# Kernel tuning notes

Measured on AMD Instinct MI355X. Metric: run time of the kernel, lower is better.

## Reference

```python
import jax, jax.numpy as jnp
import numpy as np

N_NODES = 10000
N_EDGES = 320000
IN_DIM = 128
HID = 256


def setup_inputs() -> dict:
    key = jax.random.key(0)
    ks = jax.random.split(key, 10)
    s_in = 1.0 / np.sqrt(IN_DIM)
    s_h = 1.0 / np.sqrt(HID)
    return {
        "x": jax.random.normal(ks[0], (N_NODES, IN_DIM), dtype=jnp.float32),
        "edge_index": jax.random.randint(ks[1], (2, N_EDGES), 0, N_NODES, dtype=jnp.int64),
        # feature_projector Linear(IN_DIM -> HID)
        "Wp": jax.random.uniform(ks[2], (IN_DIM, HID), jnp.float32, -s_in, s_in),
        "bp": jax.random.uniform(ks[3], (HID,), jnp.float32, -s_in, s_in),
        # LSTM(input=HID, hidden=HID) params, torch layout [4H, H], gate order i,f,g,o
        "W_ih": jax.random.uniform(ks[4], (4 * HID, HID), jnp.float32, -s_h, s_h),
        "W_hh": jax.random.uniform(ks[5], (4 * HID, HID), jnp.float32, -s_h, s_h),
        "b_ih": jax.random.uniform(ks[6], (4 * HID,), jnp.float32, -s_h, s_h),
        "b_hh": jax.random.uniform(ks[7], (4 * HID,), jnp.float32, -s_h, s_h),
        # EvolveGCN-O initial weight [H, H] (glorot-style)
        "initial_weight": jax.random.normal(ks[8], (HID, HID), dtype=jnp.float32) * np.sqrt(2.0 / (2 * HID)),
        # GCNConv bias
        "b_gcn": jnp.zeros((HID,), dtype=jnp.float32),
    }


def _forward(x, edge_index, Wp, bp, W_ih, W_hh, b_ih, b_hh, initial_weight, b_gcn):
    n = x.shape[0]
    # 1) feature projection
    h = x @ Wp + bp  # [N, H]
    # 2) EvolveGCN-O: one LSTM step on the weight matrix (rows = batch),
    #    with h0 = c0 = initial_weight; evolved hidden state is the GCN weight.
    gates = initial_weight @ W_ih.T + b_ih + initial_weight @ W_hh.T + b_hh  # [H, 4H]
    i_g, f_g, g_g, o_g = jnp.split(gates, 4, axis=-1)
    c = jax.nn.sigmoid(f_g) * initial_weight + jax.nn.sigmoid(i_g) * jnp.tanh(g_g)
    W = jax.nn.sigmoid(o_g) * jnp.tanh(c)  # [H, H]
    # 3) GCN propagation with fixed W: out = D^{-1/2}(A+I)D^{-1/2} (h W) + b
    hw = h @ W  # [N, H]
    self_loop = jnp.arange(n, dtype=edge_index.dtype)
    src = jnp.concatenate([edge_index[0], self_loop])
    dst = jnp.concatenate([edge_index[1], self_loop])
    ones = jnp.ones(src.shape[0], dtype=hw.dtype)
    deg = jax.ops.segment_sum(ones, dst, num_segments=n)  # in-degree incl. self loop
    dinv = jnp.where(deg > 0, jax.lax.rsqrt(deg), 0.0)
    norm = dinv[src] * dinv[dst]  # [E+N]
    out = jax.ops.segment_sum(hw[src] * norm[:, None], dst, num_segments=n)
    return out + b_gcn


def reference(x, edge_index, Wp, bp, W_ih, W_hh, b_ih, b_hh, initial_weight, b_gcn):
    return _forward(x, edge_index, Wp, bp, W_ih, W_hh, b_ih, b_hh, initial_weight, b_gcn)
```

## Files before the change

kernel.cpp:

```cpp
#include <hip/hip_runtime.h>
#include <math.h>

#define N_NODES 10000
#define N_EDGES 320000
#define IN_DIM  128
#define HID     256
#define CAP     128
#define NWB     64
#define NXB     128
#define NFB     448
#define NBB     (NXB + NFB)

typedef __attribute__((ext_vector_type(8))) short frag_ab;
typedef __attribute__((ext_vector_type(4))) float frag_cd;


__device__ __forceinline__ unsigned bf16rne(float f) {
    union { float f; unsigned u; } c; c.f = f;
    return (c.u + 0x7FFFu + ((c.u >> 16) & 1u)) >> 16;
}
__device__ __forceinline__ float sig_f(float x)  { return 1.f / (1.f + __expf(-x)); }
__device__ __forceinline__ float tanh_f(float x) { return 1.f - 2.f / (1.f + __expf(2.f * x)); }

__global__ __launch_bounds__(256, 2)
void k_w(const float* __restrict__ Wp, const float* __restrict__ bp,
         const float* __restrict__ wih, const float* __restrict__ whh,
         const float* __restrict__ b_ih, const float* __restrict__ b_hh,
         const float* __restrict__ iw,
         unsigned* __restrict__ wct, float* __restrict__ bc) {
    __shared__ __align__(16) char smem_raw[57920];
    const int bid = blockIdx.x;
    const int t = threadIdx.x;

    float (*aT)[260]  = (float(*)[260])smem_raw;
    float (*bSt)[20]  = (float(*)[20])(smem_raw + 33280);
    float (*iwc)[260] = (float(*)[260])(smem_raw + 53760);
    #pragma unroll
    for (int n = 0; n < 16; ++n) {
        int nrow = (n >> 2) * 256 + 4 * bid + (n & 3);
        bSt[t][n] = wih[nrow * 256 + t] + whh[nrow * 256 + t];
    }
    const int mg = t >> 2, ng = t & 3;
    const int srow = t >> 3, sf4 = t & 7;
    float acc[4][4] = {};
    for (int kt = 0; kt < 8; ++kt) {
        int k0 = kt * 32;
        __syncthreads();
        #pragma unroll
        for (int rr = 0; rr < 8; ++rr) {
            int row = srow + 32 * rr;
            float4 v = *(const float4*)&iw[row * 256 + k0 + 4 * sf4];
            aT[4 * sf4 + 0][row] = v.x; aT[4 * sf4 + 1][row] = v.y;
            aT[4 * sf4 + 2][row] = v.z; aT[4 * sf4 + 3][row] = v.w;
        }
        __syncthreads();
        if (kt == (bid >> 3)) {
            int c0 = (4 * bid) & 31;
            #pragma unroll
            for (int jj = 0; jj < 4; ++jj) iwc[jj][t] = aT[c0 + jj][t];
        }
        #pragma unroll 4
        for (int kk = 0; kk < 32; ++kk) {
            float4 a4 = *(const float4*)&aT[kk][4 * mg];
            float4 b4 = *(const float4*)&bSt[k0 + kk][4 * ng];
            float a[4] = {a4.x, a4.y, a4.z, a4.w};
            float b[4] = {b4.x, b4.y, b4.z, b4.w};
            #pragma unroll
            for (int i = 0; i < 4; ++i)
                #pragma unroll
                for (int j = 0; j < 4; ++j)
                    acc[i][j] = fmaf(a[i], b[j], acc[i][j]);
        }
    }
    float (*gates_lds)[17] = (float(*)[17])smem_raw;
    float (*wevc)[260]     = (float(*)[260])(smem_raw + 33280);
    __syncthreads();
    #pragma unroll
    for (int i = 0; i < 4; ++i)
        #pragma unroll
        for (int j = 0; j < 4; ++j)
            gates_lds[4 * mg + i][4 * ng + j] = acc[i][j];
    __syncthreads();
    {
        int r = t;
        #pragma unroll
        for (int jj = 0; jj < 4; ++jj) {
            int jcol = 4 * bid + jj;
            float gi = gates_lds[r][0  + jj] + b_ih[jcol]       + b_hh[jcol];
            float gf = gates_lds[r][4  + jj] + b_ih[256 + jcol] + b_hh[256 + jcol];
            float gg = gates_lds[r][8  + jj] + b_ih[512 + jcol] + b_hh[512 + jcol];
            float go = gates_lds[r][12 + jj] + b_ih[768 + jcol] + b_hh[768 + jcol];
            float c  = sig_f(gf) * iwc[jj][r] + sig_f(gi) * tanh_f(gg);
            wevc[jj][r] = sig_f(go) * tanh_f(c);
        }
    }
    float (*wpT)[132] = (float(*)[132])smem_raw;
    const int a2 = t & 63, jj = t >> 6;
    float c0 = 0.f, c1 = 0.f;
    for (int kt2 = 0; kt2 < 8; ++kt2) {
        int k0 = kt2 * 32;
        __syncthreads();
        #pragma unroll
        for (int ri = 0; ri < 4; ++ri) {
            int a = srow + 32 * ri;
            float4 v = *(const float4*)&Wp[a * 256 + k0 + 4 * sf4];
            wpT[4 * sf4 + 0][a] = v.x; wpT[4 * sf4 + 1][a] = v.y;
            wpT[4 * sf4 + 2][a] = v.z; wpT[4 * sf4 + 3][a] = v.w;
        }
        __syncthreads();
        #pragma unroll 8
        for (int kk = 0; kk < 32; ++kk) {
            float2 wv = *(const float2*)&wpT[kk][2 * a2];
            float wev = wevc[jj][k0 + kk];
            c0 = fmaf(wv.x, wev, c0);
            c1 = fmaf(wv.y, wev, c1);
        }
    }
    wct[(4 * bid + jj) * 64 + a2] = bf16rne(c0) | (bf16rne(c1) << 16);
    if (t < 4) {
        float s = 0.f;
        #pragma unroll 4
        for (int k4 = 0; k4 < 64; ++k4) {
            float4 b4 = *(const float4*)&bp[4 * k4];
            float4 w4 = *(const float4*)&wevc[t][4 * k4];
            s = fmaf(b4.x, w4.x, fmaf(b4.y, w4.y, fmaf(b4.z, w4.z, fmaf(b4.w, w4.w, s))));
        }
        bc[4 * bid + t] = s;
    }
}

__global__ __launch_bounds__(256)
void k_b(const float* __restrict__ x, const int* __restrict__ ei,
         int* __restrict__ cursor, unsigned* __restrict__ xb,
         int* __restrict__ bucket) {
    const int bid = blockIdx.x;
    const int t = threadIdx.x;
    if (bid < NXB) {
        const float4* x4 = (const float4*)x;
        uint2* xb2 = (uint2*)xb;
        for (int idx = bid * 256 + t; idx < N_NODES * 32; idx += NXB * 256) {
            float4 v = x4[idx];
            xb2[idx] = make_uint2(bf16rne(v.x) | (bf16rne(v.y) << 16),
                                  bf16rne(v.z) | (bf16rne(v.w) << 16));
        }
    } else {
        for (int u = (bid - NXB) * 256 + t; u < N_EDGES / 4; u += NFB * 256) {
            int4 s4 = *(const int4*)&ei[u * 4];
            int4 d4 = *(const int4*)&ei[N_EDGES + u * 4];
            int p0 = atomicAdd(&cursor[d4.x], 1);
            if (p0 < CAP) bucket[d4.x * CAP + p0] = s4.x;
            int p1 = atomicAdd(&cursor[d4.y], 1);
            if (p1 < CAP) bucket[d4.y * CAP + p1] = s4.y;
            int p2 = atomicAdd(&cursor[d4.z], 1);
            if (p2 < CAP) bucket[d4.z * CAP + p2] = s4.z;
            int p3 = atomicAdd(&cursor[d4.w], 1);
            if (p3 < CAP) bucket[d4.w * CAP + p3] = s4.w;
        }
    }
}

__global__ __launch_bounds__(256)
void k_agg(const unsigned* __restrict__ xb, const int* __restrict__ cursor,
           const int* __restrict__ bucket, unsigned* __restrict__ yb,
           float* __restrict__ rs) {
    const int t = threadIdx.x;
    const int wv = t >> 6, lane = t & 63;
    const int v = blockIdx.x * 4 + wv;
    int cntv = cursor[v];
    float dv = rsqrtf((float)(cntv + 1));
    int cnt2 = cntv > CAP ? CAP : cntv;
    unsigned self = xb[v * 64 + lane];
    union { unsigned u; float f; } c0, c1;
    c0.u = self << 16; c1.u = self & 0xFFFF0000u;
    float acc0 = dv * c0.f, acc1 = dv * c1.f, wsum = dv;
    const int4* bkt4 = (const int4*)&bucket[v * CAP];
    int j = 0;
    for (; j + 8 <= cnt2; j += 8) {
        int4 sa = bkt4[j >> 2];
        int4 sb = bkt4[(j >> 2) + 1];
        float w0 = rsqrtf((float)(cursor[sa.x] + 1));
        float w1 = rsqrtf((float)(cursor[sa.y] + 1));
        float w2 = rsqrtf((float)(cursor[sa.z] + 1));
        float w3 = rsqrtf((float)(cursor[sa.w] + 1));
        float w4 = rsqrtf((float)(cursor[sb.x] + 1));
        float w5 = rsqrtf((float)(cursor[sb.y] + 1));
        float w6 = rsqrtf((float)(cursor[sb.z] + 1));
        float w7 = rsqrtf((float)(cursor[sb.w] + 1));
        unsigned r0 = xb[sa.x * 64 + lane];
        unsigned r1 = xb[sa.y * 64 + lane];
        unsigned r2 = xb[sa.z * 64 + lane];
        unsigned r3 = xb[sa.w * 64 + lane];
        unsigned r4 = xb[sb.x * 64 + lane];
        unsigned r5 = xb[sb.y * 64 + lane];
        unsigned r6 = xb[sb.z * 64 + lane];
        unsigned r7 = xb[sb.w * 64 + lane];
        union { unsigned u; float f; } a0, a1;
        a0.u = r0 << 16; a1.u = r0 & 0xFFFF0000u;
        acc0 = fmaf(w0, a0.f, acc0); acc1 = fmaf(w0, a1.f, acc1);
        a0.u = r1 << 16; a1.u = r1 & 0xFFFF0000u;
        acc0 = fmaf(w1, a0.f, acc0); acc1 = fmaf(w1, a1.f, acc1);
        a0.u = r2 << 16; a1.u = r2 & 0xFFFF0000u;
        acc0 = fmaf(w2, a0.f, acc0); acc1 = fmaf(w2, a1.f, acc1);
        a0.u = r3 << 16; a1.u = r3 & 0xFFFF0000u;
        acc0 = fmaf(w3, a0.f, acc0); acc1 = fmaf(w3, a1.f, acc1);
        a0.u = r4 << 16; a1.u = r4 & 0xFFFF0000u;
        acc0 = fmaf(w4, a0.f, acc0); acc1 = fmaf(w4, a1.f, acc1);
        a0.u = r5 << 16; a1.u = r5 & 0xFFFF0000u;
        acc0 = fmaf(w5, a0.f, acc0); acc1 = fmaf(w5, a1.f, acc1);
        a0.u = r6 << 16; a1.u = r6 & 0xFFFF0000u;
        acc0 = fmaf(w6, a0.f, acc0); acc1 = fmaf(w6, a1.f, acc1);
        a0.u = r7 << 16; a1.u = r7 & 0xFFFF0000u;
        acc0 = fmaf(w7, a0.f, acc0); acc1 = fmaf(w7, a1.f, acc1);
        wsum += w0 + w1 + w2 + w3 + w4 + w5 + w6 + w7;
    }
    for (; j < cnt2; ++j) {
        int s = bucket[v * CAP + j];
        float ws = rsqrtf((float)(cursor[s] + 1));
        unsigned rr = xb[s * 64 + lane];
        union { unsigned u; float f; } a0, a1;
        a0.u = rr << 16; a1.u = rr & 0xFFFF0000u;
        acc0 = fmaf(ws, a0.f, acc0); acc1 = fmaf(ws, a1.f, acc1);
        wsum += ws;
    }
    yb[v * 64 + lane] = bf16rne(dv * acc0) | (bf16rne(dv * acc1) << 16);
    if (lane == 0) rs[v] = dv * wsum;
}

__global__ __launch_bounds__(256)
void k_out(const unsigned* __restrict__ yb, const unsigned* __restrict__ wct,
           const float* __restrict__ bc, const float* __restrict__ rs,
           const float* __restrict__ b_gcn, float* __restrict__ out) {
    int m0 = blockIdx.x * 16;
    int w = threadIdx.x >> 6, lane = threadIdx.x & 63;
    int q = lane >> 4, ln = lane & 15;
    const int4* yb4  = (const int4*)yb;
    const int4* wct4 = (const int4*)wct;
    union { int4 v; frag_ab f; } a[4];
    #pragma unroll
    for (int kc = 0; kc < 4; ++kc)
        a[kc].v = yb4[(m0 + ln) * 16 + kc * 4 + q];
    float rsv[4];
    #pragma unroll
    for (int r = 0; r < 4; ++r) rsv[r] = rs[m0 + q * 4 + r];
    #pragma unroll
    for (int i = 0; i < 4; ++i) {
        int n0 = (w + 4 * i) * 16;
        union { int4 v; frag_ab f; } b[4];
        #pragma unroll
        for (int kc = 0; kc < 4; ++kc)
            b[kc].v = wct4[(n0 + ln) * 16 + kc * 4 + q];
        frag_cd acc = {0.f, 0.f, 0.f, 0.f};
        #pragma unroll
        for (int kc = 0; kc < 4; ++kc)
            acc = __builtin_amdgcn_mfma_f32_16x16x32_bf16(a[kc].f, b[kc].f, acc, 0, 0, 0);
        int n = n0 + ln;
        float bcv = bc[n], bgv = b_gcn[n];
        #pragma unroll
        for (int r = 0; r < 4; ++r) {
            int m = m0 + q * 4 + r;
            out[m * HID + n] = acc[r] + rsv[r] * bcv + bgv;
        }
    }
}

extern "C" void kernel_launch(void* const* d_in, const int* in_sizes, int n_in,
                              void* d_out, int out_size, void* d_ws, size_t ws_size,
                              hipStream_t stream) {
    const float* x     = (const float*)d_in[0];
    const int*   ei    = (const int*)d_in[1];
    const float* Wp    = (const float*)d_in[2];
    const float* bp    = (const float*)d_in[3];
    const float* W_ih  = (const float*)d_in[4];
    const float* W_hh  = (const float*)d_in[5];
    const float* b_ih  = (const float*)d_in[6];
    const float* b_hh  = (const float*)d_in[7];
    const float* iw    = (const float*)d_in[8];
    const float* b_gcn = (const float*)d_in[9];
    float* out = (float*)d_out;

    char* ws = (char*)d_ws;
    int*      cursor = (int*)     (ws + 0);
    unsigned* wct    = (unsigned*)(ws + 40064);
    float*    bc     = (float*)   (ws + 105600);
    unsigned* xb     = (unsigned*)(ws + 106624);
    unsigned* yb     = (unsigned*)(ws + 2666624);
    float*    rs     = (float*)   (ws + 5226624);
    int*      bucket = (int*)     (ws + 5266624);

    hipMemsetAsync(cursor, 0, N_NODES * sizeof(int), stream);

    k_w  <<<NWB, 256, 0, stream>>>(Wp, bp, W_ih, W_hh, b_ih, b_hh, iw, wct, bc);
    k_b  <<<NBB, 256, 0, stream>>>(x, ei, cursor, xb, bucket);
    k_agg<<<2500, 256, 0, stream>>>(xb, cursor, bucket, yb, rs);
    k_out<<<625, 256, 0, stream>>>(yb, wct, bc, rs, b_gcn, out);
}
```

Before: 155.7 us.

## Fuse weight-evolution kernel into aggregation launch as extra blocks

The separate weight-evolution kernel is merged into the aggregation kernel: the first 64 blocks compute the LSTM-evolved weight and the combined projection, and the remaining blocks do the neighbor aggregation. This removes one kernel launch and lets the small weight computation overlap with the gather work. The weight path is also restructured with smaller shared-memory tiles (16-wide k steps, per-thread 16-column gate accumulators held in registers) so the fused kernel fits at higher occupancy (launch bounds 256,5). The trade-off is more register pressure in the weight blocks and a tail risk if those 64 blocks run longer than the aggregation blocks.

```diff
diff --git a/kernel.cpp b/kernel.cpp
--- a/kernel.cpp
+++ b/kernel.cpp
@@ -22,117 +22,10 @@
 __device__ __forceinline__ float sig_f(float x)  { return 1.f / (1.f + __expf(-x)); }
 __device__ __forceinline__ float tanh_f(float x) { return 1.f - 2.f / (1.f + __expf(2.f * x)); }
 
-__global__ __launch_bounds__(256, 2)
-void k_w(const float* __restrict__ Wp, const float* __restrict__ bp,
-         const float* __restrict__ wih, const float* __restrict__ whh,
-         const float* __restrict__ b_ih, const float* __restrict__ b_hh,
-         const float* __restrict__ iw,
-         unsigned* __restrict__ wct, float* __restrict__ bc) {
-    __shared__ __align__(16) char smem_raw[57920];
-    const int bid = blockIdx.x;
-    const int t = threadIdx.x;
-
-    float (*aT)[260]  = (float(*)[260])smem_raw;
-    float (*bSt)[20]  = (float(*)[20])(smem_raw + 33280);
-    float (*iwc)[260] = (float(*)[260])(smem_raw + 53760);
-    #pragma unroll
-    for (int n = 0; n < 16; ++n) {
-        int nrow = (n >> 2) * 256 + 4 * bid + (n & 3);
-        bSt[t][n] = wih[nrow * 256 + t] + whh[nrow * 256 + t];
-    }
-    const int mg = t >> 2, ng = t & 3;
-    const int srow = t >> 3, sf4 = t & 7;
-    float acc[4][4] = {};
-    for (int kt = 0; kt < 8; ++kt) {
-        int k0 = kt * 32;
-        __syncthreads();
-        #pragma unroll
-        for (int rr = 0; rr < 8; ++rr) {
-            int row = srow + 32 * rr;
-            float4 v = *(const float4*)&iw[row * 256 + k0 + 4 * sf4];
-            aT[4 * sf4 + 0][row] = v.x; aT[4 * sf4 + 1][row] = v.y;
-            aT[4 * sf4 + 2][row] = v.z; aT[4 * sf4 + 3][row] = v.w;
-        }
-        __syncthreads();
-        if (kt == (bid >> 3)) {
-            int c0 = (4 * bid) & 31;
-            #pragma unroll
-            for (int jj = 0; jj < 4; ++jj) iwc[jj][t] = aT[c0 + jj][t];
-        }
-        #pragma unroll 4
-        for (int kk = 0; kk < 32; ++kk) {
-            float4 a4 = *(const float4*)&aT[kk][4 * mg];
-            float4 b4 = *(const float4*)&bSt[k0 + kk][4 * ng];
-            float a[4] = {a4.x, a4.y, a4.z, a4.w};
-            float b[4] = {b4.x, b4.y, b4.z, b4.w};
-            #pragma unroll
-            for (int i = 0; i < 4; ++i)
-                #pragma unroll
-                for (int j = 0; j < 4; ++j)
-                    acc[i][j] = fmaf(a[i], b[j], acc[i][j]);
-        }
-    }
-    float (*gates_lds)[17] = (float(*)[17])smem_raw;
-    float (*wevc)[260]     = (float(*)[260])(smem_raw + 33280);
-    __syncthreads();
-    #pragma unroll
-    for (int i = 0; i < 4; ++i)
-        #pragma unroll
-        for (int j = 0; j < 4; ++j)
-            gates_lds[4 * mg + i][4 * ng + j] = acc[i][j];
-    __syncthreads();
-    {
-        int r = t;
-        #pragma unroll
-        for (int jj = 0; jj < 4; ++jj) {
-            int jcol = 4 * bid + jj;
-            float gi = gates_lds[r][0  + jj] + b_ih[jcol]       + b_hh[jcol];
-            float gf = gates_lds[r][4  + jj] + b_ih[256 + jcol] + b_hh[256 + jcol];
-            float gg = gates_lds[r][8  + jj] + b_ih[512 + jcol] + b_hh[512 + jcol];
-            float go = gates_lds[r][12 + jj] + b_ih[768 + jcol] + b_hh[768 + jcol];
-            float c  = sig_f(gf) * iwc[jj][r] + sig_f(gi) * tanh_f(gg);
-            wevc[jj][r] = sig_f(go) * tanh_f(c);
-        }
-    }
-    float (*wpT)[132] = (float(*)[132])smem_raw;
-    const int a2 = t & 63, jj = t >> 6;
-    float c0 = 0.f, c1 = 0.f;
-    for (int kt2 = 0; kt2 < 8; ++kt2) {
-        int k0 = kt2 * 32;
-        __syncthreads();
-        #pragma unroll
-        for (int ri = 0; ri < 4; ++ri) {
-            int a = srow + 32 * ri;
-            float4 v = *(const float4*)&Wp[a * 256 + k0 + 4 * sf4];
-            wpT[4 * sf4 + 0][a] = v.x; wpT[4 * sf4 + 1][a] = v.y;
-            wpT[4 * sf4 + 2][a] = v.z; wpT[4 * sf4 + 3][a] = v.w;
-        }
-        __syncthreads();
-        #pragma unroll 8
-        for (int kk = 0; kk < 32; ++kk) {
-            float2 wv = *(const float2*)&wpT[kk][2 * a2];
-            float wev = wevc[jj][k0 + kk];
-            c0 = fmaf(wv.x, wev, c0);
-            c1 = fmaf(wv.y, wev, c1);
-        }
-    }
-    wct[(4 * bid + jj) * 64 + a2] = bf16rne(c0) | (bf16rne(c1) << 16);
-    if (t < 4) {
-        float s = 0.f;
-        #pragma unroll 4
-        for (int k4 = 0; k4 < 64; ++k4) {
-            float4 b4 = *(const float4*)&bp[4 * k4];
-            float4 w4 = *(const float4*)&wevc[t][4 * k4];
-            s = fmaf(b4.x, w4.x, fmaf(b4.y, w4.y, fmaf(b4.z, w4.z, fmaf(b4.w, w4.w, s))));
-        }
-        bc[4 * bid + t] = s;
-    }
-}
-
 __global__ __launch_bounds__(256)
-void k_b(const float* __restrict__ x, const int* __restrict__ ei,
-         int* __restrict__ cursor, unsigned* __restrict__ xb,
-         int* __restrict__ bucket) {
+void k_fx(const float* __restrict__ x, const int* __restrict__ ei,
+          int* __restrict__ cursor, unsigned* __restrict__ xb,
+          int* __restrict__ bucket) {
     const int bid = blockIdx.x;
     const int t = threadIdx.x;
     if (bid < NXB) {
@@ -159,71 +52,162 @@
     }
 }
 
-__global__ __launch_bounds__(256)
-void k_agg(const unsigned* __restrict__ xb, const int* __restrict__ cursor,
-           const int* __restrict__ bucket, unsigned* __restrict__ yb,
-           float* __restrict__ rs) {
+__global__ __launch_bounds__(256, 5)
+void k_wagg(const float* __restrict__ Wp, const float* __restrict__ bp,
+            const float* __restrict__ wih, const float* __restrict__ whh,
+            const float* __restrict__ b_ih, const float* __restrict__ b_hh,
+            const float* __restrict__ iw,
+            const unsigned* __restrict__ xb, const int* __restrict__ cursor,
+            const int* __restrict__ bucket,
+            unsigned* __restrict__ wct, float* __restrict__ bc,
+            unsigned* __restrict__ yb, float* __restrict__ rs) {
+    __shared__ __align__(16) char smem_raw[21760];
+    const int bid = blockIdx.x;
     const int t = threadIdx.x;
-    const int wv = t >> 6, lane = t & 63;
-    const int v = blockIdx.x * 4 + wv;
-    int cntv = cursor[v];
-    float dv = rsqrtf((float)(cntv + 1));
-    int cnt2 = cntv > CAP ? CAP : cntv;
-    unsigned self = xb[v * 64 + lane];
-    union { unsigned u; float f; } c0, c1;
-    c0.u = self << 16; c1.u = self & 0xFFFF0000u;
-    float acc0 = dv * c0.f, acc1 = dv * c1.f, wsum = dv;
-    const int4* bkt4 = (const int4*)&bucket[v * CAP];
-    int j = 0;
-    for (; j + 8 <= cnt2; j += 8) {
-        int4 sa = bkt4[j >> 2];
-        int4 sb = bkt4[(j >> 2) + 1];
-        float w0 = rsqrtf((float)(cursor[sa.x] + 1));
-        float w1 = rsqrtf((float)(cursor[sa.y] + 1));
-        float w2 = rsqrtf((float)(cursor[sa.z] + 1));
-        float w3 = rsqrtf((float)(cursor[sa.w] + 1));
-        float w4 = rsqrtf((float)(cursor[sb.x] + 1));
-        float w5 = rsqrtf((float)(cursor[sb.y] + 1));
-        float w6 = rsqrtf((float)(cursor[sb.z] + 1));
-        float w7 = rsqrtf((float)(cursor[sb.w] + 1));
-        unsigned r0 = xb[sa.x * 64 + lane];
-        unsigned r1 = xb[sa.y * 64 + lane];
-        unsigned r2 = xb[sa.z * 64 + lane];
-        unsigned r3 = xb[sa.w * 64 + lane];
-        unsigned r4 = xb[sb.x * 64 + lane];
-        unsigned r5 = xb[sb.y * 64 + lane];
-        unsigned r6 = xb[sb.z * 64 + lane];
-        unsigned r7 = xb[sb.w * 64 + lane];
-        union { unsigned u; float f; } a0, a1;
-        a0.u = r0 << 16; a1.u = r0 & 0xFFFF0000u;
-        acc0 = fmaf(w0, a0.f, acc0); acc1 = fmaf(w0, a1.f, acc1);
-        a0.u = r1 << 16; a1.u = r1 & 0xFFFF0000u;
-        acc0 = fmaf(w1, a0.f, acc0); acc1 = fmaf(w1, a1.f, acc1);
-        a0.u = r2 << 16; a1.u = r2 & 0xFFFF0000u;
-        acc0 = fmaf(w2, a0.f, acc0); acc1 = fmaf(w2, a1.f, acc1);
-        a0.u = r3 << 16; a1.u = r3 & 0xFFFF0000u;
-        acc0 = fmaf(w3, a0.f, acc0); acc1 = fmaf(w3, a1.f, acc1);
-        a0.u = r4 << 16; a1.u = r4 & 0xFFFF0000u;
-        acc0 = fmaf(w4, a0.f, acc0); acc1 = fmaf(w4, a1.f, acc1);
-        a0.u = r5 << 16; a1.u = r5 & 0xFFFF0000u;
-        acc0 = fmaf(w5, a0.f, acc0); acc1 = fmaf(w5, a1.f, acc1);
-        a0.u = r6 << 16; a1.u = r6 & 0xFFFF0000u;
-        acc0 = fmaf(w6, a0.f, acc0); acc1 = fmaf(w6, a1.f, acc1);
-        a0.u = r7 << 16; a1.u = r7 & 0xFFFF0000u;
-        acc0 = fmaf(w7, a0.f, acc0); acc1 = fmaf(w7, a1.f, acc1);
-        wsum += w0 + w1 + w2 + w3 + w4 + w5 + w6 + w7;
+
+    if (bid < NWB) {
+        const int b = bid;
+        float (*aT)[256]   = (float(*)[256])smem_raw;
+        float (*bS)[20]    = (float(*)[20])(smem_raw + 16384);
+        float (*wevc)[256] = (float(*)[256])(smem_raw + 17664);
+        float gacc[16] = {};
+        float riw[4];
+        const int c0 = (4 * b) & 15, ktiw = (4 * b) >> 4;
+        for (int kt = 0; kt < 16; ++kt) {
+            int k0 = kt * 16;
+            __syncthreads();
+            #pragma unroll
+            for (int rr = 0; rr < 4; ++rr) {
+                int row = (t >> 2) + 64 * rr;
+                int kq = t & 3;
+                float4 v = *(const float4*)&iw[row * 256 + k0 + 4 * kq];
+                aT[4 * kq + 0][row] = v.x; aT[4 * kq + 1][row] = v.y;
+                aT[4 * kq + 2][row] = v.z; aT[4 * kq + 3][row] = v.w;
+            }
+            {
+                int n = t >> 4, kk = t & 15;
+                int nrow = (n >> 2) * 256 + 4 * b + (n & 3);
+                bS[kk][n] = wih[nrow * 256 + k0 + kk] + whh[nrow * 256 + k0 + kk];
+            }
+            __syncthreads();
+            if (kt == ktiw) {
+                #pragma unroll
+                for (int jj = 0; jj < 4; ++jj) riw[jj] = aT[c0 + jj][t];
+            }
+            #pragma unroll
+            for (int kk = 0; kk < 16; ++kk) {
+                float a = aT[kk][t];
+                #pragma unroll
+                for (int n = 0; n < 16; ++n)
+                    gacc[n] = fmaf(a, bS[kk][n], gacc[n]);
+            }
+        }
+        #pragma unroll
+        for (int jj = 0; jj < 4; ++jj) {
+            int jcol = 4 * b + jj;
+            float gi = gacc[0 + jj]  + b_ih[jcol]       + b_hh[jcol];
+            float gf = gacc[4 + jj]  + b_ih[256 + jcol] + b_hh[256 + jcol];
+            float gg = gacc[8 + jj]  + b_ih[512 + jcol] + b_hh[512 + jcol];
+            float go = gacc[12 + jj] + b_ih[768 + jcol] + b_hh[768 + jcol];
+            float c  = sig_f(gf) * riw[jj] + sig_f(gi) * tanh_f(gg);
+            wevc[jj][t] = sig_f(go) * tanh_f(c);
+        }
+        float (*wpT)[128] = (float(*)[128])smem_raw;
+        const int a2 = t & 63, jj = t >> 6;
+        float cc0 = 0.f, cc1 = 0.f;
+        for (int kt = 0; kt < 16; ++kt) {
+            int k0 = kt * 16;
+            __syncthreads();
+            #pragma unroll
+            for (int h = 0; h < 2; ++h) {
+                int item = t + 256 * h;
+                int a = item >> 2, ch = item & 3;
+                float4 v = *(const float4*)&Wp[a * 256 + k0 + 4 * ch];
+                wpT[4 * ch + 0][a] = v.x; wpT[4 * ch + 1][a] = v.y;
+                wpT[4 * ch + 2][a] = v.z; wpT[4 * ch + 3][a] = v.w;
+            }
+            __syncthreads();
+            #pragma unroll
+            for (int kk = 0; kk < 16; ++kk) {
+                float2 wv = *(const float2*)&wpT[kk][2 * a2];
+                float wev = wevc[jj][k0 + kk];
+                cc0 = fmaf(wv.x, wev, cc0);
+                cc1 = fmaf(wv.y, wev, cc1);
+            }
+        }
+        wct[(4 * b + jj) * 64 + a2] = bf16rne(cc0) | (bf16rne(cc1) << 16);
+        if (t < 4) {
+            float s = 0.f;
+            #pragma unroll 4
+            for (int k4 = 0; k4 < 64; ++k4) {
+                float4 b4 = *(const float4*)&bp[4 * k4];
+                float4 w4 = *(const float4*)&wevc[t][4 * k4];
+                s = fmaf(b4.x, w4.x, fmaf(b4.y, w4.y, fmaf(b4.z, w4.z, fmaf(b4.w, w4.w, s))));
+            }
+            bc[4 * b + t] = s;
+        }
+    } else {
+        const int wv = t >> 6, lane = t & 63;
+        const int v = (bid - NWB) * 4 + wv;
+        int cntv = cursor[v];
+        float dv = rsqrtf((float)(cntv + 1));
+        int cnt2 = cntv > CAP ? CAP : cntv;
+        unsigned self = xb[v * 64 + lane];
+        union { unsigned u; float f; } c0u, c1u;
+        c0u.u = self << 16; c1u.u = self & 0xFFFF0000u;
+        float acc0 = dv * c0u.f, acc1 = dv * c1u.f, wsum = dv;
+        const int4* bkt4 = (const int4*)&bucket[v * CAP];
+        int j = 0;
+        for (; j + 8 <= cnt2; j += 8) {
+            int4 sa = bkt4[j >> 2];
+            int4 sb = bkt4[(j >> 2) + 1];
+            float w0 = rsqrtf((float)(cursor[sa.x] + 1));
+            float w1 = rsqrtf((float)(cursor[sa.y] + 1));
+            float w2 = rsqrtf((float)(cursor[sa.z] + 1));
+            float w3 = rsqrtf((float)(cursor[sa.w] + 1));
+            float w4 = rsqrtf((float)(cursor[sb.x] + 1));
+            float w5 = rsqrtf((float)(cursor[sb.y] + 1));
+            float w6 = rsqrtf((float)(cursor[sb.z] + 1));
+            float w7 = rsqrtf((float)(cursor[sb.w] + 1));
+            unsigned r0 = xb[sa.x * 64 + lane];
+            unsigned r1 = xb[sa.y * 64 + lane];
+            unsigned r2 = xb[sa.z * 64 + lane];
+            unsigned r3 = xb[sa.w * 64 + lane];
+            unsigned r4 = xb[sb.x * 64 + lane];
+            unsigned r5 = xb[sb.y * 64 + lane];
+            unsigned r6 = xb[sb.z * 64 + lane];
+            unsigned r7 = xb[sb.w * 64 + lane];
+            union { unsigned u; float f; } a0, a1;
+            a0.u = r0 << 16; a1.u = r0 & 0xFFFF0000u;
+            acc0 = fmaf(w0, a0.f, acc0); acc1 = fmaf(w0, a1.f, acc1);
+            a0.u = r1 << 16; a1.u = r1 & 0xFFFF0000u;
+            acc0 = fmaf(w1, a0.f, acc0); acc1 = fmaf(w1, a1.f, acc1);
+            a0.u = r2 << 16; a1.u = r2 & 0xFFFF0000u;
+            acc0 = fmaf(w2, a0.f, acc0); acc1 = fmaf(w2, a1.f, acc1);
+            a0.u = r3 << 16; a1.u = r3 & 0xFFFF0000u;
+            acc0 = fmaf(w3, a0.f, acc0); acc1 = fmaf(w3, a1.f, acc1);
+            a0.u = r4 << 16; a1.u = r4 & 0xFFFF0000u;
+            acc0 = fmaf(w4, a0.f, acc0); acc1 = fmaf(w4, a1.f, acc1);
+            a0.u = r5 << 16; a1.u = r5 & 0xFFFF0000u;
+            acc0 = fmaf(w5, a0.f, acc0); acc1 = fmaf(w5, a1.f, acc1);
+            a0.u = r6 << 16; a1.u = r6 & 0xFFFF0000u;
+            acc0 = fmaf(w6, a0.f, acc0); acc1 = fmaf(w6, a1.f, acc1);
+            a0.u = r7 << 16; a1.u = r7 & 0xFFFF0000u;
+            acc0 = fmaf(w7, a0.f, acc0); acc1 = fmaf(w7, a1.f, acc1);
+            wsum += w0 + w1 + w2 + w3 + w4 + w5 + w6 + w7;
+        }
+        for (; j < cnt2; ++j) {
+            int s = bucket[v * CAP + j];
+            float ws = rsqrtf((float)(cursor[s] + 1));
+            unsigned rr = xb[s * 64 + lane];
+            union { unsigned u; float f; } a0, a1;
+            a0.u = rr << 16; a1.u = rr & 0xFFFF0000u;
+            acc0 = fmaf(ws, a0.f, acc0); acc1 = fmaf(ws, a1.f, acc1);
+            wsum += ws;
+        }
+        yb[v * 64 + lane] = bf16rne(dv * acc0) | (bf16rne(dv * acc1) << 16);
+        if (lane == 0) rs[v] = dv * wsum;
     }
-    for (; j < cnt2; ++j) {
-        int s = bucket[v * CAP + j];
-        float ws = rsqrtf((float)(cursor[s] + 1));
-        unsigned rr = xb[s * 64 + lane];
-        union { unsigned u; float f; } a0, a1;
-        a0.u = rr << 16; a1.u = rr & 0xFFFF0000u;
-        acc0 = fmaf(ws, a0.f, acc0); acc1 = fmaf(ws, a1.f, acc1);
-        wsum += ws;
-    }
-    yb[v * 64 + lane] = bf16rne(dv * acc0) | (bf16rne(dv * acc1) << 16);
-    if (lane == 0) rs[v] = dv * wsum;
 }
 
 __global__ __launch_bounds__(256)
@@ -289,8 +273,8 @@
 
     hipMemsetAsync(cursor, 0, N_NODES * sizeof(int), stream);
 
-    k_w  <<<NWB, 256, 0, stream>>>(Wp, bp, W_ih, W_hh, b_ih, b_hh, iw, wct, bc);
-    k_b  <<<NBB, 256, 0, stream>>>(x, ei, cursor, xb, bucket);
-    k_agg<<<2500, 256, 0, stream>>>(xb, cursor, bucket, yb, rs);
-    k_out<<<625, 256, 0, stream>>>(yb, wct, bc, rs, b_gcn, out);
-}
+    k_fx  <<<NBB, 256, 0, stream>>>(x, ei, cursor, xb, bucket);
+    k_wagg<<<NWB + 2500, 256, 0, stream>>>(Wp, bp, W_ih, W_hh, b_ih, b_hh, iw,
+                                           xb, cursor, bucket, wct, bc, yb, rs);
+    k_out <<<625, 256, 0, stream>>>(yb, wct, bc, rs, b_gcn, out);
+}
```

New measurement: 148.7 us. -4.5%, faster.
